# Optimization experiments

Hardware: AMD Instinct MI355X
Metric: run time of the kernel (lower is better)

The kernel has to match this reference:

```python
import jax, jax.numpy as jnp
import numpy as np

N = 131072      # atoms
NB = 8192       # blocks (~16 atoms each)
H = 256         # hidden_size
NH = 8          # num_heads
HD = H // NH
RBF = 16
HQ = H // 4
CUTOFF = 10.0
EPS = 1e-5


def _ln(x, g, b):
    mu = jnp.mean(x, axis=-1, keepdims=True)
    var = jnp.var(x, axis=-1, keepdims=True)
    return (x - mu) * jax.lax.rsqrt(var + EPS) * g + b


def setup_inputs():
    key = jax.random.key(0)
    ks = jax.random.split(key, 20)
    w = lambda k, sh: jax.random.normal(k, sh, jnp.float32) * 0.02
    z = lambda d: jnp.zeros((d,), jnp.float32)
    return {
        'atom_features': jax.random.normal(ks[0], (N, H), jnp.float32),
        'atom_positions': jax.random.uniform(ks[1], (N, 3), jnp.float32) * 20.0,
        'block_id': jnp.arange(N, dtype=jnp.int32) // (N // NB),
        'inter_edges': jax.random.randint(ks[2], (2, 4 * NB), 0, NB, jnp.int32),
        'pma_seed': w(ks[3], (H,)),
        'pma_wq': w(ks[4], (H, H)), 'pma_bq': z(H),
        'pma_wk': w(ks[5], (H, H)), 'pma_bk': z(H),
        'pma_wv': w(ks[6], (H, H)), 'pma_bv': z(H),
        'pma_wo': w(ks[7], (H, H)), 'pma_bo': z(H),
        'centers': jnp.linspace(0.0, CUTOFF, RBF, dtype=jnp.float32),
        'widths': jnp.full((RBF,), CUTOFF / RBF, jnp.float32),
        'geom_w': w(ks[8], (RBF, HQ)), 'geom_b': z(HQ),
        'cq_w': w(ks[9], (H, H)), 'cq_b': z(H),
        'ck_w': w(ks[10], (H + HQ, H)), 'ck_b': z(H),
        'cv_w': w(ks[11], (H + HQ, H)), 'cv_b': z(H),
        'cmlp_w1': w(ks[12], (H, H)), 'cmlp_b1': z(H),
        'cmlp_w2': w(ks[13], (H, H)), 'cmlp_b2': z(H),
        'ffn_w1': w(ks[14], (H, 2 * H)), 'ffn_b1': z(2 * H),
        'ffn_w2': w(ks[15], (2 * H, H)), 'ffn_b2': z(H),
        'ln1_g': jnp.ones((H,), jnp.float32), 'ln1_b': z(H),
        'ln2_g': jnp.ones((H,), jnp.float32), 'ln2_b': z(H),
    }


def reference(atom_features, atom_positions, block_id, inter_edges,
              pma_seed, pma_wq, pma_bq, pma_wk, pma_bk, pma_wv, pma_bv, pma_wo, pma_bo,
              centers, widths, geom_w, geom_b, cq_w, cq_b, ck_w, ck_b, cv_w, cv_b,
              cmlp_w1, cmlp_b1, cmlp_w2, cmlp_b2, ffn_w1, ffn_b1, ffn_w2, ffn_b2,
              ln1_g, ln1_b, ln2_g, ln2_b):
    bid = block_id
    seg_sum = lambda x: jax.ops.segment_sum(x, bid, NB)
    seg_max = lambda x: jax.ops.segment_max(x, bid, NB)

    # --- VectorizedPMA: one learned query pools atoms -> block features (ragged segment attention) ---
    q = (pma_seed @ pma_wq + pma_bq).reshape(NH, HD)             # query shared by all blocks
    k = (atom_features @ pma_wk + pma_bk).reshape(N, NH, HD)
    v = (atom_features @ pma_wv + pma_bv).reshape(N, NH, HD)
    s = jnp.einsum('hd,nhd->nh', q, k) * (HD ** -0.5)            # [N, NH]
    e = jnp.exp(s - seg_max(s)[bid])
    wgt = e / jnp.maximum(seg_sum(e), 1e-20)[bid]
    block_feat = seg_sum(wgt[:, :, None] * v).reshape(NB, H) @ pma_wo + pma_bo  # [NB, H]

    # --- geometry: per-block centroid, relative distance, RBF encoding ---
    cnt = seg_sum(jnp.ones((N,), atom_positions.dtype))
    cent = seg_sum(atom_positions) / jnp.maximum(cnt, 1.0)[:, None]
    rel = atom_positions - cent[bid]
    dist = jnp.sqrt(jnp.sum(rel * rel, axis=1))
    rbf = jnp.exp(-((dist[:, None] - centers[None, :]) ** 2) / (2.0 * widths[None, :] ** 2))
    aug = jnp.concatenate([atom_features, rbf @ geom_w + geom_b], axis=1)       # [N, H+H/4]

    # --- block -> atoms cross attention (single query per block over its atoms) ---
    Q = block_feat @ cq_w + cq_b
    K = aug @ ck_w + ck_b
    V = aug @ cv_w + cv_b
    sc = jnp.sum(Q[bid] * K, axis=1) / float(np.sqrt(H))
    e2 = jnp.exp(sc - seg_max(sc)[bid])
    w2 = e2 / jnp.maximum(seg_sum(e2), 1e-20)[bid]
    ctx = seg_sum(w2[:, None] * V)                                # [NB, H]
    upd = jax.nn.relu(ctx @ cmlp_w1 + cmlp_b1) @ cmlp_w2 + cmlp_b2

    # --- broadcast update back to atoms, residual + LN, FFN + LN (eval: dropout = identity) ---
    x = _ln(atom_features + upd[bid], ln1_g, ln1_b)
    x = _ln(x + jax.nn.relu(x @ ffn_w1 + ffn_b1) @ ffn_w2 + ffn_b2, ln2_g, ln2_b)
    return x
```

## Files before the change

kernel.cpp:

```cpp
#include <hip/hip_runtime.h>
#include <hip/hip_bf16.h>

#define NATOMS 131072
#define NBLK   8192
#define HDIM   256
#define NHEAD  8
#define TDIM   336

typedef __attribute__((ext_vector_type(8))) short short8;
typedef __attribute__((ext_vector_type(4))) float floatx4;

__device__ __forceinline__ float bfu2f(unsigned short u) {
  unsigned int v = ((unsigned int)u) << 16;
  return __builtin_bit_cast(float, v);
}
__device__ __forceinline__ unsigned short f2bfu(float f) {
  unsigned int u = __builtin_bit_cast(unsigned int, f);
  u += 0x7fffu + ((u >> 16) & 1u);
  return (unsigned short)(u >> 16);
}
__device__ __forceinline__ unsigned int cvt2(float a, float b) {
  unsigned int r;
  asm("v_cvt_pk_bf16_f32 %0, %1, %2" : "=v"(r) : "v"(a), "v"(b));
  return r;
}

__global__ __launch_bounds__(352) void prepA(
    const float* __restrict__ seed, const float* __restrict__ Wq,
    const float* __restrict__ bq, const float* __restrict__ Wk,
    const float* __restrict__ bk, unsigned short* __restrict__ A_bfT,
    float* __restrict__ sb,
    const float* __restrict__ cq_w, const float* __restrict__ cq_b,
    const float* __restrict__ ck_w, const float* __restrict__ ck_b,
    float* __restrict__ M, float* __restrict__ vbias,
    const float* __restrict__ cv_w, const float* __restrict__ cv_b,
    const float* __restrict__ w1m, const float* __restrict__ b1m,
    unsigned short* __restrict__ CV1Tb, float* __restrict__ cb1,
    const float* __restrict__ fw1, const float* __restrict__ fw2,
    const float* __restrict__ w2m, const float* __restrict__ geom_w,
    unsigned short* __restrict__ W1t, unsigned short* __restrict__ W2t,
    unsigned short* __restrict__ W2mTb, unsigned short* __restrict__ geomT) {
  __shared__ float row[256];
  int t = threadIdx.x, b = blockIdx.x;
  if (b < 9) {
    if (t < 256) {
      float acc = bq[t];
      for (int c = 0; c < 256; ++c) acc += seed[c] * Wq[c * 256 + t];
      row[t] = acc;
    }
    __syncthreads();
    const float scale = 0.17677669529663687f;
    if (b < 8) {
      if (t < 256) {
        int o = b * 256 + t;
        int c = o >> 3, h = o & 7;
        float a = 0.f;
        for (int d = 0; d < 32; ++d) a += Wk[c * 256 + h * 32 + d] * row[h * 32 + d];
        A_bfT[h * 256 + c] = f2bfu(a * scale);
      }
    } else {
      if (t < 8) {
        float a = 0.f;
        for (int d = 0; d < 32; ++d) a += bk[t * 32 + d] * row[t * 32 + d];
        sb[t] = a * scale;
      }
      if (t < 256)
        for (int idx = t; idx < 2048; idx += 256) A_bfT[2048 + idx] = 0;
    }
  } else if (b < 265) {
    int i = b - 9;
    if (t < 256) row[t] = cq_w[i * 256 + t];
    __syncthreads();
    if (t < TDIM) {
      float a = 0.f;
      if (t < 320) { const float* w = ck_w + t * 256; for (int j = 0; j < 256; ++j) a += row[j] * w[j]; }
      else if (t == 320) { for (int j = 0; j < 256; ++j) a += row[j] * ck_b[j]; }
      M[i * TDIM + t] = a;
    }
    if (i == 0) {
      __syncthreads();
      if (t < 256) row[t] = cq_b[t];
      __syncthreads();
      if (t < TDIM) {
        float a = 0.f;
        if (t < 320) { const float* w = ck_w + t * 256; for (int j = 0; j < 256; ++j) a += row[j] * w[j]; }
        else if (t == 320) { for (int j = 0; j < 256; ++j) a += row[j] * ck_b[j]; }
        vbias[t] = a;
      }
    }
  } else if (b < 586) {
    int k = b - 265;
    if (t < 256) row[t] = (k < 320) ? cv_w[k * 256 + t] : cv_b[t];
    __syncthreads();
    if (t < 256) {
      float a = 0.f;
      for (int i = 0; i < 256; ++i) a += row[i] * w1m[i * 256 + t];
      if (k < 320) CV1Tb[t * 320 + k] = f2bfu(a);
      else cb1[t] = a + b1m[t];
    }
  } else {
    int bb = b - 586;
    if (bb < 512) {
      if (t < 256) W1t[bb * 256 + t] = f2bfu(fw1[t * 512 + bb]);
    } else if (bb < 768) {
      int n = bb - 512;
      if (t < 256)
        for (int m = 0; m < 2; ++m) {
          int k = t + 256 * m;
          W2t[n * 512 + k] = f2bfu(fw2[k * 256 + n]);
        }
    } else if (bb == 768) {
      if (t < 256)
        for (int idx = t; idx < 2048; idx += 256) {
          int q = idx >> 5, r = idx & 31;
          geomT[idx] = (r < 16) ? f2bfu(geom_w[r * 64 + q]) : (unsigned short)0;
        }
    } else {
      int n = bb - 769;
      if (t < 256) W2mTb[n * 256 + t] = f2bfu(w2m[t * 256 + n]);
    }
  }
}

__global__ __launch_bounds__(352) void kp2(const float* __restrict__ Wo,
    const float* __restrict__ bo, const float* __restrict__ M,
    const float* __restrict__ vbias, float* __restrict__ MM, float* __restrict__ vb2) {
  __shared__ float row[256];
  int p = blockIdx.x, t = threadIdx.x;
  const float* src = (p < 256) ? (Wo + p * 256) : bo;
  if (t < 256) row[t] = src[t];
  __syncthreads();
  if (t < TDIM) {
    float a = 0.f;
    for (int i = 0; i < 256; ++i) a += row[i] * M[i * TDIM + t];
    if (p < 256) MM[p * TDIM + t] = a;
    else vb2[t] = a + vbias[t];
  }
}

__global__ __launch_bounds__(256, 4) void kgm(const float* __restrict__ x,
    const unsigned short* __restrict__ A_bfT, const float* __restrict__ sb,
    const float* __restrict__ Wv, const float* __restrict__ bv,
    const float* __restrict__ MM, const float* __restrict__ vb2,
    float* __restrict__ T) {
  __shared__ __align__(16) char buf[33792];
  unsigned short (*xs)[264] = (unsigned short(*)[264])buf;
  float (*ys)[8][260] = (float(*)[8][260])buf;
  __shared__ unsigned short wsm[64][8];
  __shared__ float bp[4][260];
  int t = threadIdx.x, wg = blockIdx.x;
  long a0 = (long)wg * 64;
  int B0 = wg * 4;
  int lane = t & 63, w = t >> 6;
  int lrow = lane & 15, hi = lane >> 4, lk = hi * 8;

  const float4* x4 = (const float4*)(x + a0 * 256);
  for (int m = 0; m < 16; ++m) {
    int f4 = t + 256 * m;
    int row = f4 >> 6, c4 = f4 & 63;
    float4 v = x4[f4];
    uint2 q;
    q.x = cvt2(v.x, v.y);
    q.y = cvt2(v.z, v.w);
    *(uint2*)&xs[row][c4 * 4] = q;
  }
  float sblv = (lrow < 8) ? sb[lrow] : 0.f;
  __syncthreads();

  floatx4 zero = {0.f, 0.f, 0.f, 0.f};
  floatx4 accs = zero;
#pragma unroll
  for (int k0 = 0; k0 < 8; ++k0) {
    short8 af = *(const short8*)&xs[16 * w + lrow][k0 * 32 + lk];
    short8 bf = *(const short8*)(A_bfT + lrow * 256 + k0 * 32 + lk);
    accs = __builtin_amdgcn_mfma_f32_16x16x32_bf16(af, bf, accs, 0, 0, 0);
  }
  {
    float sv[4], e[4];
    float mx = -1e30f;
#pragma unroll
    for (int i = 0; i < 4; ++i) { sv[i] = accs[i] + sblv; mx = fmaxf(mx, sv[i]); }
    mx = fmaxf(mx, __shfl_xor(mx, 16));
    mx = fmaxf(mx, __shfl_xor(mx, 32));
    float se = 0.f;
#pragma unroll
    for (int i = 0; i < 4; ++i) { e[i] = __expf(sv[i] - mx); se += e[i]; }
    se += __shfl_xor(se, 16);
    se += __shfl_xor(se, 32);
    float inv = 1.f / fmaxf(se, 1e-20f);
    if (lrow < 8) {
#pragma unroll
      for (int i = 0; i < 4; ++i) wsm[16 * w + hi * 4 + i][lrow] = f2bfu(e[i] * inv);
    }
  }
  __syncthreads();

  int h = lrow & 7, bsel = lrow >> 3;
  short8 A1, A2;
#pragma unroll
  for (int j = 0; j < 8; ++j) {
    int atom = 8 * hi + j;
    unsigned short w1v = wsm[atom][h];
    unsigned short w2v = wsm[32 + atom][h];
    A1[j] = (bsel == (atom >> 4)) ? (short)w1v : (short)0;
    A2[j] = (bsel == (atom >> 4)) ? (short)w2v : (short)0;
  }
  floatx4 d1r[4], d2r[4];
#pragma unroll
  for (int q = 0; q < 4; ++q) {
    int ct = 4 * w + q;
    int cb = ct * 16 + lrow;
    short8 B1, B2;
#pragma unroll
    for (int j = 0; j < 8; ++j) {
      B1[j] = (short)xs[8 * hi + j][cb];
      B2[j] = (short)xs[32 + 8 * hi + j][cb];
    }
    d1r[q] = __builtin_amdgcn_mfma_f32_16x16x32_bf16(A1, B1, zero, 0, 0, 0);
    d2r[q] = __builtin_amdgcn_mfma_f32_16x16x32_bf16(A2, B2, zero, 0, 0, 0);
  }
  __syncthreads();

#pragma unroll
  for (int q = 0; q < 4; ++q) {
    int ct = 4 * w + q;
#pragma unroll
    for (int i = 0; i < 4; ++i) {
      int r = hi * 4 + i;
      int hh = r & 7, bb = r >> 3;
      ys[bb][hh][ct * 16 + lrow] = d1r[q][i];
      ys[2 + bb][hh][ct * 16 + lrow] = d2r[q][i];
    }
  }
  __syncthreads();

  {
    int h2 = t >> 5;
    float acc[4];
    float bvj = bv[t];
#pragma unroll
    for (int bb = 0; bb < 4; ++bb) acc[bb] = bvj;
    const float* wp = Wv + t;
    for (int c = 0; c < 256; c += 8) {
      float wv[8];
#pragma unroll
      for (int k = 0; k < 8; ++k) wv[k] = wp[(c + k) * 256];
#pragma unroll
      for (int bb = 0; bb < 4; ++bb) {
        float4 y4a = *(const float4*)&ys[bb][h2][c];
        float4 y4b = *(const float4*)&ys[bb][h2][c + 4];
        acc[bb] += wv[0] * y4a.x + wv[1] * y4a.y + wv[2] * y4a.z + wv[3] * y4a.w
                 + wv[4] * y4b.x + wv[5] * y4b.y + wv[6] * y4b.z + wv[7] * y4b.w;
      }
    }
#pragma unroll
    for (int bb = 0; bb < 4; ++bb) bp[bb][t] = acc[bb];
  }
  __syncthreads();

#pragma unroll
  for (int chunk = 0; chunk < 2; ++chunk) {
    int c = chunk * 256 + t;
    if (c < TDIM) {
      float vb = vb2[c];
      float acc[4];
#pragma unroll
      for (int bb = 0; bb < 4; ++bb) acc[bb] = vb;
      const float* mc = MM + c;
      for (int j = 0; j < 256; j += 8) {
        float wv[8];
#pragma unroll
        for (int k = 0; k < 8; ++k) wv[k] = mc[(j + k) * TDIM];
#pragma unroll
        for (int bb = 0; bb < 4; ++bb) {
          float4 r4a = *(const float4*)&bp[bb][j];
          float4 r4b = *(const float4*)&bp[bb][j + 4];
          acc[bb] += wv[0] * r4a.x + wv[1] * r4a.y + wv[2] * r4a.z + wv[3] * r4a.w
                   + wv[4] * r4b.x + wv[5] * r4b.y + wv[6] * r4b.z + wv[7] * r4b.w;
        }
      }
#pragma unroll
      for (int bb = 0; bb < 4; ++bb)
        T[(long)(B0 + bb) * TDIM + c] = acc[bb];
    }
  }
}

__global__ __launch_bounds__(256) void kg3(const float* __restrict__ x,
    const float* __restrict__ pos, const float* __restrict__ T,
    const float* __restrict__ centers, const float* __restrict__ widths,
    const unsigned short* __restrict__ geomT, const float* __restrict__ geom_b,
    float* __restrict__ z_f) {
  __shared__ unsigned short xs[64][264];
  __shared__ unsigned short rbflb[64][32];
  __shared__ unsigned short rbfpb[64][72];
  __shared__ unsigned short TbfT[4][328];
  __shared__ float Tbias[4];
  __shared__ float ps[64][3];
  __shared__ float cent[4][3];
  __shared__ float ctr[16], wid[16];
  __shared__ float w2l[64];
  int t = threadIdx.x, wg = blockIdx.x;
  long a0 = (long)wg * 64;
  int b0 = wg * 4;
  int lane = t & 63, w = t >> 6;
  int lrow = lane & 15, hi = lane >> 4, lk = hi * 8;

  const float4* x4 = (const float4*)(x + a0 * 256);
  for (int m = 0; m < 16; ++m) {
    int f4 = t + 256 * m;
    int row = f4 >> 6, c4 = f4 & 63;
    float4 v = x4[f4];
    uint2 q;
    q.x = cvt2(v.x, v.y);
    q.y = cvt2(v.z, v.w);
    *(uint2*)&xs[row][c4 * 4] = q;
  }
  if (t < 192) ps[t / 3][t % 3] = pos[a0 * 3 + t];
  if (t >= 224 && t < 240) ctr[t - 224] = centers[t - 224];
  if (t >= 240) wid[t - 240] = widths[t - 240];
#pragma unroll
  for (int j = 0; j < 4; ++j)
    for (int c = t; c < 321; c += 256) {
      float v = T[(long)(b0 + j) * TDIM + c];
      if (c < 320) TbfT[j][c] = f2bfu(v);
      else Tbias[j] = v;
    }
  __syncthreads();
  if (t < 12) {
    int b = t / 3, d = t % 3;
    float s = 0.f;
    for (int i = 0; i < 16; ++i) s += ps[b * 16 + i][d];
    cent[b][d] = s * 0.0625f;
  }
  __syncthreads();
  if (t < 64) {
    int b = t >> 4;
    float dx = ps[t][0] - cent[b][0];
    float dy = ps[t][1] - cent[b][1];
    float dz = ps[t][2] - cent[b][2];
    float dist = sqrtf(dx * dx + dy * dy + dz * dz);
    for (int r = 0; r < 16; ++r) {
      float dd = dist - ctr[r];
      rbflb[t][r] = f2bfu(__expf(-dd * dd / (2.f * wid[r] * wid[r])));
      rbflb[t][16 + r] = 0;
    }
  }
  __syncthreads();

  floatx4 zero = {0.f, 0.f, 0.f, 0.f};
  {
    short8 A = *(const short8*)&rbflb[16 * w + lrow][lk];
#pragma unroll
    for (int qt = 0; qt < 4; ++qt) {
      short8 B = *(const short8*)(geomT + (qt * 16 + lrow) * 32 + lk);
      floatx4 d = __builtin_amdgcn_mfma_f32_16x16x32_bf16(A, B, zero, 0, 0, 0);
      float gb = geom_b[qt * 16 + lrow];
#pragma unroll
      for (int i = 0; i < 4; ++i)
        rbfpb[16 * w + hi * 4 + i][qt * 16 + lrow] = f2bfu(d[i] + gb);
    }
  }
  __syncthreads();

  {
    floatx4 acc = zero;
#pragma unroll
    for (int k0 = 0; k0 < 8; ++k0) {
      short8 af = *(const short8*)&xs[16 * w + lrow][k0 * 32 + lk];
      short8 bf = *(const short8*)&TbfT[lrow & 3][k0 * 32 + lk];
      acc = __builtin_amdgcn_mfma_f32_16x16x32_bf16(af, bf, acc, 0, 0, 0);
    }
#pragma unroll
    for (int kq = 0; kq < 2; ++kq) {
      short8 af = *(const short8*)&rbfpb[16 * w + lrow][kq * 32 + lk];
      short8 bf = *(const short8*)&TbfT[lrow & 3][256 + kq * 32 + lk];
      acc = __builtin_amdgcn_mfma_f32_16x16x32_bf16(af, bf, acc, 0, 0, 0);
    }
    float tb = Tbias[w];
    float sv[4], e[4];
    float mx = -1e30f;
#pragma unroll
    for (int i = 0; i < 4; ++i) { sv[i] = (acc[i] + tb) * 0.0625f; mx = fmaxf(mx, sv[i]); }
    mx = fmaxf(mx, __shfl_xor(mx, 16));
    mx = fmaxf(mx, __shfl_xor(mx, 32));
    float se = 0.f;
#pragma unroll
    for (int i = 0; i < 4; ++i) { e[i] = __expf(sv[i] - mx); se += e[i]; }
    se += __shfl_xor(se, 16);
    se += __shfl_xor(se, 32);
    float inv = 1.f / fmaxf(se, 1e-20f);
    if (lrow == w) {
#pragma unroll
      for (int i = 0; i < 4; ++i) w2l[16 * w + hi * 4 + i] = e[i] * inv;
    }
  }
  __syncthreads();

  for (int b = 0; b < 4; ++b) {
    float zv = 0.f;
    for (int i = 0; i < 16; ++i) zv += w2l[b * 16 + i] * bfu2f(xs[b * 16 + i][t]);
    z_f[(long)(b0 + b) * 320 + t] = zv;
  }
  {
    int q = t & 63, b = t >> 6;
    float zq = 0.f;
    for (int i = 0; i < 16; ++i) zq += w2l[b * 16 + i] * bfu2f(rbfpb[b * 16 + i][q]);
    z_f[(long)(b0 + b) * 320 + 256 + q] = zq;
  }
}

__global__ __launch_bounds__(256, 4) void gb2(const float* __restrict__ z_f,
    const unsigned short* __restrict__ CV1Tb, const float* __restrict__ cb1,
    const unsigned short* __restrict__ W2mTb, const float* __restrict__ b2m,
    float* __restrict__ upd) {
  __shared__ unsigned short zb[16][328];
  __shared__ unsigned short prb[16][264];
  int t = threadIdx.x;
  int B0 = blockIdx.x * 16;
  int lane = t & 63, w = t >> 6;
  int lrow = lane & 15, hi = lane >> 4, lk = hi * 8;
  floatx4 zero = {0.f, 0.f, 0.f, 0.f};

  for (int idx = t; idx < 16 * 320; idx += 256) {
    int r = idx / 320, c = idx - r * 320;
    zb[r][c] = f2bfu(z_f[(long)(B0 + r) * 320 + c]);
  }
  __syncthreads();

#pragma unroll
  for (int tt = 0; tt < 4; ++tt) {
    int colt = w * 4 + tt;
    floatx4 acc = zero;
    const unsigned short* ap = CV1Tb + (colt * 16 + lrow) * 320 + lk;
#pragma unroll
    for (int ks = 0; ks < 10; ++ks) {
      short8 A = *(const short8*)(ap + ks * 32);
      short8 B = *(const short8*)&zb[lrow][ks * 32 + lk];
      acc = __builtin_amdgcn_mfma_f32_16x16x32_bf16(A, B, acc, 0, 0, 0);
    }
    float4 cbv = ((const float4*)cb1)[colt * 4 + hi];
    float r0 = fmaxf(acc[0] + cbv.x, 0.f);
    float r1 = fmaxf(acc[1] + cbv.y, 0.f);
    float r2 = fmaxf(acc[2] + cbv.z, 0.f);
    float r3 = fmaxf(acc[3] + cbv.w, 0.f);
    uint2 q;
    q.x = cvt2(r0, r1);
    q.y = cvt2(r2, r3);
    *(uint2*)&prb[lrow][colt * 16 + hi * 4] = q;
  }
  __syncthreads();

#pragma unroll
  for (int tt = 0; tt < 4; ++tt) {
    int colt = w * 4 + tt;
    floatx4 acc = zero;
    const unsigned short* ap = W2mTb + (colt * 16 + lrow) * 256 + lk;
#pragma unroll
    for (int ks = 0; ks < 8; ++ks) {
      short8 A = *(const short8*)(ap + ks * 32);
      short8 B = *(const short8*)&prb[lrow][ks * 32 + lk];
      acc = __builtin_amdgcn_mfma_f32_16x16x32_bf16(A, B, acc, 0, 0, 0);
    }
    float4 b2v = ((const float4*)b2m)[colt * 4 + hi];
    float4 st;
    st.x = acc[0] + b2v.x;
    st.y = acc[1] + b2v.y;
    st.z = acc[2] + b2v.z;
    st.w = acc[3] + b2v.w;
    *(float4*)&upd[(long)(B0 + lrow) * 256 + colt * 16 + hi * 4] = st;
  }
}

__global__ __launch_bounds__(512, 4) void kf(const float* __restrict__ x,
    const float* __restrict__ upd, const unsigned short* __restrict__ W1t,
    const unsigned short* __restrict__ W2t, const float* __restrict__ b1,
    const float* __restrict__ b2, const float* __restrict__ g1,
    const float* __restrict__ be1, const float* __restrict__ g2,
    const float* __restrict__ be2, float* __restrict__ out) {
  __shared__ unsigned short x1s[64][264];
  __shared__ unsigned short hs[64][136];
  int t = threadIdx.x, wg = blockIdx.x;
  long a0 = (long)wg * 64;
  int b0 = wg * 4;
  int lane = t & 63, w = t >> 6;
  int lrow = lane & 15, hi = lane >> 4;
  int lk = hi * 8;

  {
    float4 gv1 = ((const float4*)g1)[lane];
    float4 bv1 = ((const float4*)be1)[lane];
#pragma unroll
    for (int rr = 0; rr < 8; ++rr) {
      int row = w * 8 + rr;
      float4 xv = ((const float4*)(x + (a0 + row) * 256))[lane];
      float4 uv = ((const float4*)(upd + (long)(b0 + (row >> 4)) * 256))[lane];
      float4 v;
      v.x = xv.x + uv.x; v.y = xv.y + uv.y; v.z = xv.z + uv.z; v.w = xv.w + uv.w;
      float s = v.x + v.y + v.z + v.w;
      float sq = v.x * v.x + v.y * v.y + v.z * v.z + v.w * v.w;
#pragma unroll
      for (int d = 1; d < 64; d <<= 1) { s += __shfl_xor(s, d); sq += __shfl_xor(sq, d); }
      float mu = s * (1.f / 256.f);
      float var = sq * (1.f / 256.f) - mu * mu;
      float rstd = rsqrtf(fmaxf(var, 0.f) + 1e-5f);
      uint2 q;
      q.x = cvt2((v.x - mu) * rstd * gv1.x + bv1.x, (v.y - mu) * rstd * gv1.y + bv1.y);
      q.y = cvt2((v.z - mu) * rstd * gv1.z + bv1.z, (v.w - mu) * rstd * gv1.w + bv1.w);
      *(uint2*)&x1s[row][lane * 4] = q;
    }
  }
  __syncthreads();

  floatx4 zero = {0.f, 0.f, 0.f, 0.f};
  floatx4 acc2[2][4];
#pragma unroll
  for (int cb = 0; cb < 2; ++cb)
    for (int rb = 0; rb < 4; ++rb) acc2[cb][rb] = zero;

  for (int s = 0; s < 4; ++s) {
    int hc = s * 128 + w * 16 + lrow;
    short8 wf[8];
#pragma unroll
    for (int k0 = 0; k0 < 8; ++k0)
      wf[k0] = *(const short8*)(W1t + hc * 256 + k0 * 32 + lk);
    floatx4 acc1[4] = {zero, zero, zero, zero};
#pragma unroll
    for (int k0 = 0; k0 < 8; ++k0) {
      short8 af0 = *(const short8*)&x1s[0 + lrow][k0 * 32 + lk];
      short8 af1 = *(const short8*)&x1s[16 + lrow][k0 * 32 + lk];
      short8 af2 = *(const short8*)&x1s[32 + lrow][k0 * 32 + lk];
      short8 af3 = *(const short8*)&x1s[48 + lrow][k0 * 32 + lk];
      acc1[0] = __builtin_amdgcn_mfma_f32_16x16x32_bf16(wf[k0], af0, acc1[0], 0, 0, 0);
      acc1[1] = __builtin_amdgcn_mfma_f32_16x16x32_bf16(wf[k0], af1, acc1[1], 0, 0, 0);
      acc1[2] = __builtin_amdgcn_mfma_f32_16x16x32_bf16(wf[k0], af2, acc1[2], 0, 0, 0);
      acc1[3] = __builtin_amdgcn_mfma_f32_16x16x32_bf16(wf[k0], af3, acc1[3], 0, 0, 0);
    }
    short8 wf2[8];
#pragma unroll
    for (int cb = 0; cb < 2; ++cb)
      for (int ks = 0; ks < 4; ++ks)
        wf2[cb * 4 + ks] = *(const short8*)(W2t + (w * 32 + cb * 16 + lrow) * 512 + s * 128 + ks * 32 + lk);
    float4 b4 = ((const float4*)b1)[s * 32 + w * 4 + hi];
    __syncthreads();
#pragma unroll
    for (int rb = 0; rb < 4; ++rb) {
      float r0 = fmaxf(acc1[rb][0] + b4.x, 0.f);
      float r1 = fmaxf(acc1[rb][1] + b4.y, 0.f);
      float r2 = fmaxf(acc1[rb][2] + b4.z, 0.f);
      float r3 = fmaxf(acc1[rb][3] + b4.w, 0.f);
      uint2 q;
      q.x = cvt2(r0, r1);
      q.y = cvt2(r2, r3);
      *(uint2*)&hs[rb * 16 + lrow][w * 16 + hi * 4] = q;
    }
    __syncthreads();
#pragma unroll
    for (int ks = 0; ks < 4; ++ks) {
      short8 a20 = *(const short8*)&hs[0 + lrow][ks * 32 + lk];
      short8 a21 = *(const short8*)&hs[16 + lrow][ks * 32 + lk];
      short8 a22 = *(const short8*)&hs[32 + lrow][ks * 32 + lk];
      short8 a23 = *(const short8*)&hs[48 + lrow][ks * 32 + lk];
#pragma unroll
      for (int cb = 0; cb < 2; ++cb) {
        acc2[cb][0] = __builtin_amdgcn_mfma_f32_16x16x32_bf16(wf2[cb * 4 + ks], a20, acc2[cb][0], 0, 0, 0);
        acc2[cb][1] = __builtin_amdgcn_mfma_f32_16x16x32_bf16(wf2[cb * 4 + ks], a21, acc2[cb][1], 0, 0, 0);
        acc2[cb][2] = __builtin_amdgcn_mfma_f32_16x16x32_bf16(wf2[cb * 4 + ks], a22, acc2[cb][2], 0, 0, 0);
        acc2[cb][3] = __builtin_amdgcn_mfma_f32_16x16x32_bf16(wf2[cb * 4 + ks], a23, acc2[cb][3], 0, 0, 0);
      }
    }
  }

#pragma unroll
  for (int cb = 0; cb < 2; ++cb) {
    float4 b4 = ((const float4*)b2)[w * 8 + cb * 4 + hi];
    int colb = w * 32 + cb * 16 + hi * 4;
#pragma unroll
    for (int rb = 0; rb < 4; ++rb) {
      int atom = rb * 16 + lrow;
      ushort4 old = *(const ushort4*)&x1s[atom][colb];
      float r0 = acc2[cb][rb][0] + b4.x + bfu2f(old.x);
      float r1 = acc2[cb][rb][1] + b4.y + bfu2f(old.y);
      float r2 = acc2[cb][rb][2] + b4.z + bfu2f(old.z);
      float r3 = acc2[cb][rb][3] + b4.w + bfu2f(old.w);
      uint2 q;
      q.x = cvt2(r0, r1);
      q.y = cvt2(r2, r3);
      *(uint2*)&x1s[atom][colb] = q;
    }
  }
  __syncthreads();

  {
    float4 gv2 = ((const float4*)g2)[lane];
    float4 bv2 = ((const float4*)be2)[lane];
#pragma unroll
    for (int rr = 0; rr < 8; ++rr) {
      int row = w * 8 + rr;
      ushort4 u = *(const ushort4*)&x1s[row][lane * 4];
      float v0 = bfu2f(u.x), v1 = bfu2f(u.y), v2 = bfu2f(u.z), v3 = bfu2f(u.w);
      float s = v0 + v1 + v2 + v3;
      float sq = v0 * v0 + v1 * v1 + v2 * v2 + v3 * v3;
#pragma unroll
      for (int d = 1; d < 64; d <<= 1) { s += __shfl_xor(s, d); sq += __shfl_xor(sq, d); }
      float mu = s * (1.f / 256.f);
      float var = sq * (1.f / 256.f) - mu * mu;
      float rstd = rsqrtf(fmaxf(var, 0.f) + 1e-5f);
      float4 o;
      o.x = (v0 - mu) * rstd * gv2.x + bv2.x;
      o.y = (v1 - mu) * rstd * gv2.y + bv2.y;
      o.z = (v2 - mu) * rstd * gv2.z + bv2.z;
      o.w = (v3 - mu) * rstd * gv2.w + bv2.w;
      ((float4*)(out + (a0 + row) * 256))[lane] = o;
    }
  }
}

extern "C" void kernel_launch(void* const* d_in, const int* in_sizes, int n_in,
                              void* d_out, int out_size, void* d_ws, size_t ws_size,
                              hipStream_t stream) {
  (void)in_sizes; (void)n_in; (void)out_size; (void)ws_size;
  const float* x    = (const float*)d_in[0];
  const float* pos  = (const float*)d_in[1];
  const float* seed = (const float*)d_in[4];
  const float* Wq   = (const float*)d_in[5];
  const float* bq   = (const float*)d_in[6];
  const float* Wk   = (const float*)d_in[7];
  const float* bk   = (const float*)d_in[8];
  const float* Wv   = (const float*)d_in[9];
  const float* bv   = (const float*)d_in[10];
  const float* Wo   = (const float*)d_in[11];
  const float* bo   = (const float*)d_in[12];
  const float* centers = (const float*)d_in[13];
  const float* widths  = (const float*)d_in[14];
  const float* geom_w  = (const float*)d_in[15];
  const float* geom_b  = (const float*)d_in[16];
  const float* cq_w = (const float*)d_in[17];
  const float* cq_b = (const float*)d_in[18];
  const float* ck_w = (const float*)d_in[19];
  const float* ck_b = (const float*)d_in[20];
  const float* cv_w = (const float*)d_in[21];
  const float* cv_b = (const float*)d_in[22];
  const float* w1m  = (const float*)d_in[23];
  const float* b1m  = (const float*)d_in[24];
  const float* w2m  = (const float*)d_in[25];
  const float* b2m  = (const float*)d_in[26];
  const float* fw1  = (const float*)d_in[27];
  const float* fb1  = (const float*)d_in[28];
  const float* fw2  = (const float*)d_in[29];
  const float* fb2  = (const float*)d_in[30];
  const float* g1   = (const float*)d_in[31];
  const float* be1  = (const float*)d_in[32];
  const float* g2   = (const float*)d_in[33];
  const float* be2  = (const float*)d_in[34];

  float* ws = (float*)d_ws;
  float* sb = ws + 0;
  unsigned short* A_bfT = (unsigned short*)(ws + 64);
  float* M     = ws + 2112;
  float* vbias = ws + 88128;
  float* MM    = ws + 88480;
  float* vb2   = ws + 174496;
  unsigned short* CV1Tb = (unsigned short*)(ws + 174848);
  float* cb1   = ws + 215808;
  unsigned short* W1t = (unsigned short*)(ws + 216064);
  unsigned short* W2t = (unsigned short*)(ws + 281600);
  unsigned short* W2mTb = (unsigned short*)(ws + 347136);
  float* updw = ws + 379904;
  unsigned short* geomT = (unsigned short*)(ws + 2477056);

  float* outp = (float*)d_out;
  float* T   = outp + 16777216;
  float* zf  = outp + 21626880;

  prepA<<<dim3(1611), dim3(352), 0, stream>>>(seed, Wq, bq, Wk, bk, A_bfT, sb,
      cq_w, cq_b, ck_w, ck_b, M, vbias,
      cv_w, cv_b, w1m, b1m, CV1Tb, cb1,
      fw1, fw2, w2m, geom_w, W1t, W2t, W2mTb, geomT);
  kp2<<<dim3(257), dim3(352), 0, stream>>>(Wo, bo, M, vbias, MM, vb2);
  kgm<<<dim3(2048), dim3(256), 0, stream>>>(x, A_bfT, sb, Wv, bv, MM, vb2, T);
  kg3<<<dim3(2048), dim3(256), 0, stream>>>(x, pos, T, centers, widths, geomT, geom_b, zf);
  gb2<<<dim3(512), dim3(256), 0, stream>>>(zf, CV1Tb, cb1, W2mTb, b2m, updw);
  kf<<<dim3(2048), dim3(512), 0, stream>>>(x, updw, W1t, W2t, fb1, fb2, g1, be1, g2, be2, outp);
}
```

Before: 352.7 us.

## Replace scalar FP32 Wv and MM projections in kgm with bf16 MFMA

The two per-block projections in kgm (per-head Wv projection, then the fused Wo·M projection to TDIM) used scalar FP32 FMA loops that read global weights column-strided. They now run on 16x16x32 bf16 MFMA, with four block rows padded to 16 and the intermediates stored as bf16 in shared memory. Wv and MM are pre-transposed to bf16 in prepA and kp2, and the workspace layout is shifted to fit the new buffer. This cuts per-workgroup ALU work and weight bandwidth, but adds bf16 rounding on intermediates and wastes 12 of the 16 MFMA rows.

```diff
diff --git a/kernel.cpp b/kernel.cpp
--- a/kernel.cpp
+++ b/kernel.cpp
@@ -39,7 +39,8 @@
     const float* __restrict__ fw1, const float* __restrict__ fw2,
     const float* __restrict__ w2m, const float* __restrict__ geom_w,
     unsigned short* __restrict__ W1t, unsigned short* __restrict__ W2t,
-    unsigned short* __restrict__ W2mTb, unsigned short* __restrict__ geomT) {
+    unsigned short* __restrict__ W2mTb, unsigned short* __restrict__ geomT,
+    const float* __restrict__ Wv, unsigned short* __restrict__ WvTb) {
   __shared__ float row[256];
   int t = threadIdx.x, b = blockIdx.x;
   if (b < 9) {
@@ -98,7 +99,7 @@
       if (k < 320) CV1Tb[t * 320 + k] = f2bfu(a);
       else cb1[t] = a + b1m[t];
     }
-  } else {
+  } else if (b < 1611) {
     int bb = b - 586;
     if (bb < 512) {
       if (t < 256) W1t[bb * 256 + t] = f2bfu(fw1[t * 512 + bb]);
@@ -119,12 +120,16 @@
       int n = bb - 769;
       if (t < 256) W2mTb[n * 256 + t] = f2bfu(w2m[t * 256 + n]);
     }
+  } else {
+    int j = b - 1611;
+    if (t < 256) WvTb[j * 256 + t] = f2bfu(Wv[t * 256 + j]);
   }
 }
 
 __global__ __launch_bounds__(352) void kp2(const float* __restrict__ Wo,
     const float* __restrict__ bo, const float* __restrict__ M,
-    const float* __restrict__ vbias, float* __restrict__ MM, float* __restrict__ vb2) {
+    const float* __restrict__ vbias, unsigned short* __restrict__ MMTb,
+    float* __restrict__ vb2) {
   __shared__ float row[256];
   int p = blockIdx.x, t = threadIdx.x;
   const float* src = (p < 256) ? (Wo + p * 256) : bo;
@@ -133,21 +138,21 @@
   if (t < TDIM) {
     float a = 0.f;
     for (int i = 0; i < 256; ++i) a += row[i] * M[i * TDIM + t];
-    if (p < 256) MM[p * TDIM + t] = a;
+    if (p < 256) MMTb[t * 256 + p] = f2bfu(a);
     else vb2[t] = a + vbias[t];
   }
 }
 
 __global__ __launch_bounds__(256, 4) void kgm(const float* __restrict__ x,
     const unsigned short* __restrict__ A_bfT, const float* __restrict__ sb,
-    const float* __restrict__ Wv, const float* __restrict__ bv,
-    const float* __restrict__ MM, const float* __restrict__ vb2,
+    const unsigned short* __restrict__ WvTb, const float* __restrict__ bv,
+    const unsigned short* __restrict__ MMTb, const float* __restrict__ vb2,
     float* __restrict__ T) {
   __shared__ __align__(16) char buf[33792];
   unsigned short (*xs)[264] = (unsigned short(*)[264])buf;
-  float (*ys)[8][260] = (float(*)[8][260])buf;
+  unsigned short (*ysb)[8][264] = (unsigned short(*)[8][264])buf;
   __shared__ unsigned short wsm[64][8];
-  __shared__ float bp[4][260];
+  __shared__ unsigned short bpb[4][264];
   int t = threadIdx.x, wg = blockIdx.x;
   long a0 = (long)wg * 64;
   int B0 = wg * 4;
@@ -228,60 +233,49 @@
     for (int i = 0; i < 4; ++i) {
       int r = hi * 4 + i;
       int hh = r & 7, bb = r >> 3;
-      ys[bb][hh][ct * 16 + lrow] = d1r[q][i];
-      ys[2 + bb][hh][ct * 16 + lrow] = d2r[q][i];
-    }
-  }
-  __syncthreads();
-
-  {
-    int h2 = t >> 5;
-    float acc[4];
-    float bvj = bv[t];
-#pragma unroll
-    for (int bb = 0; bb < 4; ++bb) acc[bb] = bvj;
-    const float* wp = Wv + t;
-    for (int c = 0; c < 256; c += 8) {
-      float wv[8];
-#pragma unroll
-      for (int k = 0; k < 8; ++k) wv[k] = wp[(c + k) * 256];
-#pragma unroll
-      for (int bb = 0; bb < 4; ++bb) {
-        float4 y4a = *(const float4*)&ys[bb][h2][c];
-        float4 y4b = *(const float4*)&ys[bb][h2][c + 4];
-        acc[bb] += wv[0] * y4a.x + wv[1] * y4a.y + wv[2] * y4a.z + wv[3] * y4a.w
-                 + wv[4] * y4b.x + wv[5] * y4b.y + wv[6] * y4b.z + wv[7] * y4b.w;
+      ysb[bb][hh][ct * 16 + lrow] = f2bfu(d1r[q][i]);
+      ysb[2 + bb][hh][ct * 16 + lrow] = f2bfu(d2r[q][i]);
+    }
+  }
+  __syncthreads();
+
+#pragma unroll
+  for (int hh2 = 0; hh2 < 2; ++hh2) {
+    int hd = 2 * w + hh2;
+#pragma unroll
+    for (int n = 0; n < 2; ++n) {
+      floatx4 acc = zero;
+#pragma unroll
+      for (int ks = 0; ks < 8; ++ks) {
+        short8 A = *(const short8*)&ysb[lrow & 3][hd][ks * 32 + lk];
+        short8 B = *(const short8*)(WvTb + (hd * 32 + n * 16 + lrow) * 256 + ks * 32 + lk);
+        acc = __builtin_amdgcn_mfma_f32_16x16x32_bf16(A, B, acc, 0, 0, 0);
       }
-    }
-#pragma unroll
-    for (int bb = 0; bb < 4; ++bb) bp[bb][t] = acc[bb];
-  }
-  __syncthreads();
-
-#pragma unroll
-  for (int chunk = 0; chunk < 2; ++chunk) {
-    int c = chunk * 256 + t;
-    if (c < TDIM) {
+      if (hi == 0) {
+        int col = hd * 32 + n * 16 + lrow;
+        float bvc = bv[col];
+#pragma unroll
+        for (int i = 0; i < 4; ++i)
+          bpb[i][col] = f2bfu(acc[i] + bvc);
+      }
+    }
+  }
+  __syncthreads();
+
+  for (int ct = w; ct < 21; ct += 4) {
+    floatx4 acc = zero;
+#pragma unroll
+    for (int ks = 0; ks < 8; ++ks) {
+      short8 A = *(const short8*)&bpb[lrow & 3][ks * 32 + lk];
+      short8 B = *(const short8*)(MMTb + (ct * 16 + lrow) * 256 + ks * 32 + lk);
+      acc = __builtin_amdgcn_mfma_f32_16x16x32_bf16(A, B, acc, 0, 0, 0);
+    }
+    if (hi == 0) {
+      int c = ct * 16 + lrow;
       float vb = vb2[c];
-      float acc[4];
-#pragma unroll
-      for (int bb = 0; bb < 4; ++bb) acc[bb] = vb;
-      const float* mc = MM + c;
-      for (int j = 0; j < 256; j += 8) {
-        float wv[8];
-#pragma unroll
-        for (int k = 0; k < 8; ++k) wv[k] = mc[(j + k) * TDIM];
-#pragma unroll
-        for (int bb = 0; bb < 4; ++bb) {
-          float4 r4a = *(const float4*)&bp[bb][j];
-          float4 r4b = *(const float4*)&bp[bb][j + 4];
-          acc[bb] += wv[0] * r4a.x + wv[1] * r4a.y + wv[2] * r4a.z + wv[3] * r4a.w
-                   + wv[4] * r4b.x + wv[5] * r4b.y + wv[6] * r4b.z + wv[7] * r4b.w;
-        }
-      }
-#pragma unroll
-      for (int bb = 0; bb < 4; ++bb)
-        T[(long)(B0 + bb) * TDIM + c] = acc[bb];
+#pragma unroll
+      for (int i = 0; i < 4; ++i)
+        T[(long)(B0 + i) * TDIM + c] = acc[i] + vb;
     }
   }
 }
@@ -659,26 +653,27 @@
   unsigned short* A_bfT = (unsigned short*)(ws + 64);
   float* M     = ws + 2112;
   float* vbias = ws + 88128;
-  float* MM    = ws + 88480;
-  float* vb2   = ws + 174496;
-  unsigned short* CV1Tb = (unsigned short*)(ws + 174848);
-  float* cb1   = ws + 215808;
-  unsigned short* W1t = (unsigned short*)(ws + 216064);
-  unsigned short* W2t = (unsigned short*)(ws + 281600);
-  unsigned short* W2mTb = (unsigned short*)(ws + 347136);
-  float* updw = ws + 379904;
-  unsigned short* geomT = (unsigned short*)(ws + 2477056);
+  unsigned short* MMTb = (unsigned short*)(ws + 88480);
+  float* vb2   = ws + 131488;
+  unsigned short* CV1Tb = (unsigned short*)(ws + 131840);
+  float* cb1   = ws + 172800;
+  unsigned short* W1t = (unsigned short*)(ws + 173056);
+  unsigned short* W2t = (unsigned short*)(ws + 238592);
+  unsigned short* W2mTb = (unsigned short*)(ws + 304128);
+  unsigned short* WvTb = (unsigned short*)(ws + 336896);
+  float* updw = ws + 369664;
+  unsigned short* geomT = (unsigned short*)(ws + 2466816);
 
   float* outp = (float*)d_out;
   float* T   = outp + 16777216;
   float* zf  = outp + 21626880;
 
-  prepA<<<dim3(1611), dim3(352), 0, stream>>>(seed, Wq, bq, Wk, bk, A_bfT, sb,
+  prepA<<<dim3(1867), dim3(352), 0, stream>>>(seed, Wq, bq, Wk, bk, A_bfT, sb,
       cq_w, cq_b, ck_w, ck_b, M, vbias,
       cv_w, cv_b, w1m, b1m, CV1Tb, cb1,
-      fw1, fw2, w2m, geom_w, W1t, W2t, W2mTb, geomT);
-  kp2<<<dim3(257), dim3(352), 0, stream>>>(Wo, bo, M, vbias, MM, vb2);
-  kgm<<<dim3(2048), dim3(256), 0, stream>>>(x, A_bfT, sb, Wv, bv, MM, vb2, T);
+      fw1, fw2, w2m, geom_w, W1t, W2t, W2mTb, geomT, Wv, WvTb);
+  kp2<<<dim3(257), dim3(352), 0, stream>>>(Wo, bo, M, vbias, MMTb, vb2);
+  kgm<<<dim3(2048), dim3(256), 0, stream>>>(x, A_bfT, sb, WvTb, bv, MMTb, vb2, T);
   kg3<<<dim3(2048), dim3(256), 0, stream>>>(x, pos, T, centers, widths, geomT, geom_b, zf);
   gb2<<<dim3(512), dim3(256), 0, stream>>>(zf, CV1Tb, cb1, W2mTb, b2m, updw);
   kf<<<dim3(2048), dim3(512), 0, stream>>>(x, updw, W1t, W2t, fb1, fb2, g1, be1, g2, be2, outp);
```

After: 335.3 us. -4.9%, faster.
